# Optimization experiments

Hardware: AMD Instinct MI355X
Metric: run time of the kernel (lower is better)

The kernel has to match this reference:

```python
import jax, jax.numpy as jnp
import numpy as np

H = 16      # num_attention_heads
HKV = 4     # num_key_value_heads
HIDDEN = 1024
HEAD_DIM = HIDDEN // H  # 64
ROPE_BASE = 10000.0


def _rope(x):
    # Rotate-half RoPE applied over the FULL projected last dim, matching the
    # module which applies self._rope before splitting into heads.
    B, S, D = x.shape
    half = D // 2
    inv_freq = 1.0 / (ROPE_BASE ** (jnp.arange(half, dtype=jnp.float32) / half))
    ang = jnp.arange(S, dtype=jnp.float32)[:, None] * inv_freq[None, :]  # [S, half]
    cos, sin = jnp.cos(ang), jnp.sin(ang)
    x1, x2 = x[..., :half], x[..., half:]
    return jnp.concatenate([x1 * cos - x2 * sin, x2 * cos + x1 * sin], axis=-1)


def _rmsnorm(x):
    # F.rms_norm with no weight: x / sqrt(mean(x^2) + eps)
    eps = jnp.finfo(x.dtype).eps
    return x * jax.lax.rsqrt(jnp.mean(x * x, axis=-1, keepdims=True) + eps)


def setup_inputs() -> dict:
    key = jax.random.key(0)
    ks = jax.random.split(key, 10)
    B, S = 2, 2048
    kv_dim = HKV * HEAD_DIM
    sc = 0.02
    return {
        "hidden_state": jax.random.normal(ks[0], (B, S, HIDDEN), dtype=jnp.float32),
        "attention_mask": jnp.zeros((B, S, S), dtype=jnp.float32),
        "Wq": jax.random.normal(ks[1], (HIDDEN, HIDDEN), dtype=jnp.float32) * sc,
        "bq": jnp.zeros((HIDDEN,), dtype=jnp.float32),
        "Wk": jax.random.normal(ks[2], (HIDDEN, kv_dim), dtype=jnp.float32) * sc,
        "bk": jnp.zeros((kv_dim,), dtype=jnp.float32),
        "Wv": jax.random.normal(ks[3], (HIDDEN, kv_dim), dtype=jnp.float32) * sc,
        "bv": jnp.zeros((kv_dim,), dtype=jnp.float32),
        "Wo": jax.random.normal(ks[4], (HIDDEN, HIDDEN), dtype=jnp.float32) * sc,
        "bo": jnp.zeros((HIDDEN,), dtype=jnp.float32),
    }


def reference(hidden_state, attention_mask, Wq, bq, Wk, bk, Wv, bv, Wo, bo):
    B, S, _ = hidden_state.shape
    G = H // HKV  # query heads per kv head
    d = HEAD_DIM

    q = hidden_state @ Wq + bq            # [B,S,H*d]
    k = hidden_state @ Wk + bk            # [B,S,Hkv*d]
    v = hidden_state @ Wv + bv            # [B,S,Hkv*d]

    q = _rope(q)
    k = _rope(k)

    # split heads; repeat_interleave of KV over groups == grouping Q heads as [Hkv, G]
    q = q.reshape(B, S, H, d).transpose(0, 2, 1, 3).reshape(B, HKV, G, S, d)
    k = k.reshape(B, S, HKV, d).transpose(0, 2, 1, 3)   # [B,Hkv,S,d]
    v = v.reshape(B, S, HKV, d).transpose(0, 2, 1, 3)   # [B,Hkv,S,d]

    q = _rmsnorm(q)
    k = _rmsnorm(k)

    scale = d ** 0.5
    scores = jnp.einsum('bkgqd,bksd->bkgqs', q, k) / scale  # [B,Hkv,G,S,S]
    scores = scores + attention_mask[:, None, None, :, :]
    attn = jax.nn.softmax(scores, axis=-1)
    out = jnp.einsum('bkgqs,bksd->bkgqd', attn, v)          # [B,Hkv,G,S,d]

    out = out.reshape(B, H, S, d).transpose(0, 2, 1, 3).reshape(B, S, H * d)
    return out @ Wo + bo
```

## Files before the change

### kernel.cpp

```cpp
#include <hip/hip_runtime.h>
#include <cmath>

#define SEQ 2048
#define BATCH 2
#define HID 1024
#define NH 16
#define NKV 4
#define DH 64
#define KVDIM 256
#define K32C 32

typedef __attribute__((ext_vector_type(8))) short bf16x8;
typedef __attribute__((ext_vector_type(4))) float f32x4;

static __device__ __forceinline__ unsigned short f2bf(float x) {
  union { float f; unsigned u; } v; v.f = x;
  unsigned r = v.u + 0x7fffu + ((v.u >> 16) & 1u);
  return (unsigned short)(r >> 16);
}
static __device__ __forceinline__ float bf2f(unsigned short h) {
  union { unsigned u; float f; } v; v.u = ((unsigned)h) << 16;
  return v.f;
}
static __device__ __forceinline__ void gl_lds16(const unsigned short* g, unsigned short* l) {
  __builtin_amdgcn_global_load_lds(
      (const __attribute__((address_space(1))) unsigned int*)g,
      (__attribute__((address_space(3))) unsigned int*)l, 16, 0, 0);
}

template<bool HILO>
__global__ __launch_bounds__(256) void pack_a_kernel(
    const float* __restrict__ A, unsigned short* __restrict__ hi,
    unsigned short* __restrict__ lo) {
  int gid = blockIdx.x * 256 + threadIdx.x;
  int lane = gid & 63;
  int k32 = (gid >> 6) & 31;
  int m16 = gid >> 11;
  int quad = lane >> 4, l16 = lane & 15;
  const float* src = A + (size_t)(m16 * 16 + l16) * 1024 + k32 * 32 + quad * 8;
  float4 a0 = *(const float4*)src;
  float4 a1 = *(const float4*)(src + 4);
  float v[8] = {a0.x, a0.y, a0.z, a0.w, a1.x, a1.y, a1.z, a1.w};
  unsigned short h[8], l[8];
#pragma unroll
  for (int j = 0; j < 8; ++j) {
    h[j] = f2bf(v[j]);
    if (HILO) l[j] = f2bf(v[j] - bf2f(h[j]));
  }
  *(bf16x8*)(hi + (size_t)gid * 8) = *(bf16x8*)h;
  if (HILO) *(bf16x8*)(lo + (size_t)gid * 8) = *(bf16x8*)l;
}

template<bool HILO>
__global__ __launch_bounds__(256) void pack_b_kernel(
    const float* __restrict__ W, unsigned short* __restrict__ hi,
    unsigned short* __restrict__ lo, int Nsrc) {
  int gid = blockIdx.x * 256 + threadIdx.x;
  int lane = gid & 63;
  int k32 = (gid >> 6) & 31;
  int n16 = gid >> 11;
  int quad = lane >> 4, l16 = lane & 15;
  int n = n16 * 16 + l16, k = k32 * 32 + quad * 8;
  unsigned short h[8], l[8];
#pragma unroll
  for (int j = 0; j < 8; ++j) {
    float v = W[(size_t)(k + j) * Nsrc + n];
    h[j] = f2bf(v);
    if (HILO) l[j] = f2bf(v - bf2f(h[j]));
  }
  *(bf16x8*)(hi + (size_t)gid * 8) = *(bf16x8*)h;
  if (HILO) *(bf16x8*)(lo + (size_t)gid * 8) = *(bf16x8*)l;
}

__global__ __launch_bounds__(256) void bias_cat_kernel(
    const float* __restrict__ bq, const float* __restrict__ bk,
    const float* __restrict__ bv, float* __restrict__ dst) {
  int n = blockIdx.x * 256 + threadIdx.x;
  if (n < 1536)
    dst[n] = (n < 1024) ? bq[n] : (n < 1280 ? bk[n - 1024] : bv[n - 1280]);
}

template<int CHAINS, bool OUTBF16>
__global__ __launch_bounds__(256) void gemm_pk_kernel(
    const unsigned short* __restrict__ Ah, const unsigned short* __restrict__ Al,
    const unsigned short* __restrict__ Bh, const unsigned short* __restrict__ Bl,
    const float* __restrict__ bias, void* __restrict__ Cout, int N) {
  constexpr int NCH = (CHAINS == 3) ? 2 : 1;
  __shared__ unsigned short Asm[NCH][4 * 512];
  __shared__ unsigned short Bsm[NCH][8 * 512];
  const int tid = threadIdx.x;
  const int wave = tid >> 6, lane = tid & 63;
  const int wr = wave >> 1, wc = wave & 1;
  const int quad = lane >> 4, l16 = lane & 15;
  const size_t abase = ((size_t)(blockIdx.y * 4 + wave) * K32C) * 64 + lane;
  const size_t bbase0 = ((size_t)(blockIdx.x * 8 + wave) * K32C) * 64 + lane;
  const size_t bbase1 = ((size_t)(blockIdx.x * 8 + wave + 4) * K32C) * 64 + lane;
  f32x4 acc[2][4] = {};
  for (int k32 = 0; k32 < K32C; ++k32) {
    __syncthreads();
    gl_lds16(Ah + (abase + (size_t)k32 * 64) * 8, &Asm[0][wave * 512]);
    gl_lds16(Bh + (bbase0 + (size_t)k32 * 64) * 8, &Bsm[0][wave * 512]);
    gl_lds16(Bh + (bbase1 + (size_t)k32 * 64) * 8, &Bsm[0][(wave + 4) * 512]);
    if (CHAINS == 3) {
      gl_lds16(Al + (abase + (size_t)k32 * 64) * 8, &Asm[1][wave * 512]);
      gl_lds16(Bl + (bbase0 + (size_t)k32 * 64) * 8, &Bsm[1][wave * 512]);
      gl_lds16(Bl + (bbase1 + (size_t)k32 * 64) * 8, &Bsm[1][(wave + 4) * 512]);
    }
    __syncthreads();
    bf16x8 af[2][NCH], bfr[4][NCH];
#pragma unroll
    for (int mt = 0; mt < 2; ++mt)
#pragma unroll
      for (int ch = 0; ch < NCH; ++ch)
        af[mt][ch] = *(const bf16x8*)&Asm[ch][((wr * 2 + mt) * 64 + lane) * 8];
#pragma unroll
    for (int nt = 0; nt < 4; ++nt)
#pragma unroll
      for (int ch = 0; ch < NCH; ++ch)
        bfr[nt][ch] = *(const bf16x8*)&Bsm[ch][((wc * 4 + nt) * 64 + lane) * 8];
#pragma unroll
    for (int mt = 0; mt < 2; ++mt)
#pragma unroll
      for (int nt = 0; nt < 4; ++nt) {
        acc[mt][nt] = __builtin_amdgcn_mfma_f32_16x16x32_bf16(af[mt][0], bfr[nt][0], acc[mt][nt], 0, 0, 0);
        if (CHAINS == 3) {
          acc[mt][nt] = __builtin_amdgcn_mfma_f32_16x16x32_bf16(af[mt][1], bfr[nt][0], acc[mt][nt], 0, 0, 0);
          acc[mt][nt] = __builtin_amdgcn_mfma_f32_16x16x32_bf16(af[mt][0], bfr[nt][1], acc[mt][nt], 0, 0, 0);
        }
      }
  }
  const int n0 = blockIdx.x * 128 + wc * 64;
  const int m0 = blockIdx.y * 64 + wr * 32;
#pragma unroll
  for (int mt = 0; mt < 2; ++mt)
#pragma unroll
    for (int nt = 0; nt < 4; ++nt)
#pragma unroll
      for (int r = 0; r < 4; ++r) {
        int gm = m0 + mt * 16 + quad * 4 + r;
        int n = n0 + nt * 16 + l16;
        float v = acc[mt][nt][r] + bias[n];
        if (OUTBF16)
          ((unsigned short*)Cout)[(size_t)gm * N + n] = f2bf(v);
        else
          ((float*)Cout)[(size_t)gm * N + n] = v;
      }
}

__global__ __launch_bounds__(1024) void rope_norm_q_kernel(
    const unsigned short* __restrict__ qkv, unsigned short* __restrict__ qnh,
    unsigned short* __restrict__ qnl) {
  const int s = blockIdx.x, b = blockIdx.y;
  const int t = threadIdx.x;
  const unsigned short* row = qkv + ((size_t)b * SEQ + s) * 1536;
  const int j = t & 511;
  float invf = exp2f((float)j * (-13.287712379549449f / 512.0f));
  float ang = (float)s * invf;
  float c = cosf(ang), sn = sinf(ang);
  float x1 = bf2f(row[j]), x2 = bf2f(row[j + 512]);
  float val = (t < 512) ? (x1 * c - x2 * sn) : (x2 * c + x1 * sn);
  float ss = val * val;
#pragma unroll
  for (int off = 1; off < 64; off <<= 1) ss += __shfl_xor(ss, off);
  float rn = rsqrtf(ss * (1.0f / 64.0f) + 1.1920929e-07f);
  float v = val * rn;
  unsigned short hi = f2bf(v);
  unsigned short lo = f2bf(v - bf2f(hi));
  int h = t >> 6, d = t & 63;
  size_t o = (((size_t)b * NH + h) * SEQ + s) * DH + d;
  qnh[o] = hi;
  qnl[o] = lo;
}

__global__ __launch_bounds__(256) void rope_norm_kv_kernel(
    const unsigned short* __restrict__ qkv, unsigned short* __restrict__ knh,
    unsigned short* __restrict__ knl, unsigned short* __restrict__ vt) {
  const int s = blockIdx.x, b = blockIdx.y;
  const int t = threadIdx.x;
  const unsigned short* row = qkv + ((size_t)b * SEQ + s) * 1536;
  const int j = t & 127;
  float invf = exp2f((float)j * (-13.287712379549449f / 128.0f));
  float ang = (float)s * invf;
  float c = cosf(ang), sn = sinf(ang);
  float x1 = bf2f(row[1024 + j]), x2 = bf2f(row[1024 + 128 + j]);
  float val = (t < 128) ? (x1 * c - x2 * sn) : (x2 * c + x1 * sn);
  float ss = val * val;
#pragma unroll
  for (int off = 1; off < 64; off <<= 1) ss += __shfl_xor(ss, off);
  float rn = rsqrtf(ss * (1.0f / 64.0f) + 1.1920929e-07f);
  float kv = val * rn;
  unsigned short hi = f2bf(kv);
  unsigned short lo = f2bf(kv - bf2f(hi));
  int h = t >> 6, d = t & 63;
  size_t o = (((size_t)b * NKV + h) * SEQ + s) * DH + d;
  knh[o] = hi;
  knl[o] = lo;
  vt[(((size_t)b * NKV + h) * DH + d) * SEQ + s] = row[1280 + t];
}

__global__ __launch_bounds__(256) void attn_mfma_kernel(
    const unsigned short* __restrict__ qnh, const unsigned short* __restrict__ qnl,
    const unsigned short* __restrict__ knh, const unsigned short* __restrict__ knl,
    const unsigned short* __restrict__ vtb, const float* __restrict__ mask,
    float* __restrict__ out) {
  __shared__ unsigned short Ksh[32][72];
  __shared__ unsigned short Ksl[32][72];
  __shared__ unsigned short Vts[64][40];
  __shared__ float Ms[32][36];
  __shared__ unsigned short Ps[4][32][40];

  const int b = blockIdx.z, kvh = blockIdx.y;
  const int q0 = blockIdx.x * 32;
  const int tid = threadIdx.x;
  const int wave = tid >> 6, lane = tid & 63;
  const int quad = lane >> 4, l16 = lane & 15;
  const int h = kvh * 4 + wave;

  bf16x8 qh[2][2], ql[2][2];
  {
    const unsigned short* qb_h = qnh + (((size_t)b * NH + h) * SEQ) * DH;
    const unsigned short* qb_l = qnl + (((size_t)b * NH + h) * SEQ) * DH;
#pragma unroll
    for (int mt = 0; mt < 2; ++mt)
#pragma unroll
      for (int kf = 0; kf < 2; ++kf) {
        size_t o = (size_t)(q0 + mt * 16 + l16) * DH + kf * 32 + quad * 8;
        qh[mt][kf] = *(const bf16x8*)(qb_h + o);
        ql[mt][kf] = *(const bf16x8*)(qb_l + o);
      }
  }

  f32x4 O[2][4] = {};
  float l_acc[2][4] = {};

  const unsigned short* Kbh = knh + ((size_t)b * NKV + kvh) * SEQ * DH;
  const unsigned short* Kbl = knl + ((size_t)b * NKV + kvh) * SEQ * DH;
  const unsigned short* Vb  = vtb + ((size_t)b * NKV + kvh) * DH * SEQ;
  const float* mbase = mask + ((size_t)b * SEQ + q0) * SEQ;

  for (int j0 = 0; j0 < SEQ; j0 += 32) {
    __syncthreads();
    {
      int j = tid >> 3, c = tid & 7;
      *(uint4*)&Ksh[j][c * 8] = *(const uint4*)(Kbh + (size_t)(j0 + j) * DH + c * 8);
      *(uint4*)&Ksl[j][c * 8] = *(const uint4*)(Kbl + (size_t)(j0 + j) * DH + c * 8);
      int d = tid >> 2, c2 = tid & 3;
      *(uint4*)&Vts[d][c2 * 8] = *(const uint4*)(Vb + (size_t)d * SEQ + j0 + c2 * 8);
      *(float4*)&Ms[j][c * 4] = *(const float4*)(mbase + (size_t)j * SEQ + j0 + c * 4);
    }
    __syncthreads();

    bf16x8 kbh[2][2], kbl[2][2];
#pragma unroll
    for (int nt = 0; nt < 2; ++nt)
#pragma unroll
      for (int kf = 0; kf < 2; ++kf) {
        kbh[nt][kf] = *(const bf16x8*)&Ksh[nt * 16 + l16][kf * 32 + quad * 8];
        kbl[nt][kf] = *(const bf16x8*)&Ksl[nt * 16 + l16][kf * 32 + quad * 8];
      }

    f32x4 C[2][2] = {};
#pragma unroll
    for (int mt = 0; mt < 2; ++mt)
#pragma unroll
      for (int nt = 0; nt < 2; ++nt) {
#pragma unroll
        for (int kf = 0; kf < 2; ++kf) {
          C[mt][nt] = __builtin_amdgcn_mfma_f32_16x16x32_bf16(qh[mt][kf], kbh[nt][kf], C[mt][nt], 0, 0, 0);
          C[mt][nt] = __builtin_amdgcn_mfma_f32_16x16x32_bf16(ql[mt][kf], kbh[nt][kf], C[mt][nt], 0, 0, 0);
          C[mt][nt] = __builtin_amdgcn_mfma_f32_16x16x32_bf16(qh[mt][kf], kbl[nt][kf], C[mt][nt], 0, 0, 0);
        }
      }

#pragma unroll
    for (int mt = 0; mt < 2; ++mt)
#pragma unroll
      for (int nt = 0; nt < 2; ++nt)
#pragma unroll
        for (int r = 0; r < 4; ++r) {
          int row = mt * 16 + quad * 4 + r;
          float p = __expf(fmaf(C[mt][nt][r], 0.125f, Ms[row][nt * 16 + l16] - 8.0f));
          l_acc[mt][r] += p;
          Ps[wave][row][nt * 16 + l16] = f2bf(p);
        }

    bf16x8 pa[2], vbf[4];
#pragma unroll
    for (int mt = 0; mt < 2; ++mt)
      pa[mt] = *(const bf16x8*)&Ps[wave][mt * 16 + l16][quad * 8];
#pragma unroll
    for (int nt = 0; nt < 4; ++nt)
      vbf[nt] = *(const bf16x8*)&Vts[nt * 16 + l16][quad * 8];
#pragma unroll
    for (int mt = 0; mt < 2; ++mt)
#pragma unroll
      for (int nt = 0; nt < 4; ++nt)
        O[mt][nt] = __builtin_amdgcn_mfma_f32_16x16x32_bf16(pa[mt], vbf[nt], O[mt][nt], 0, 0, 0);
  }

#pragma unroll
  for (int mt = 0; mt < 2; ++mt)
#pragma unroll
    for (int r = 0; r < 4; ++r) {
#pragma unroll
      for (int off = 1; off < 16; off <<= 1)
        l_acc[mt][r] += __shfl_xor(l_acc[mt][r], off);
    }

#pragma unroll
  for (int mt = 0; mt < 2; ++mt)
#pragma unroll
    for (int r = 0; r < 4; ++r) {
      float inv = 1.0f / l_acc[mt][r];
      int s = q0 + mt * 16 + quad * 4 + r;
#pragma unroll
      for (int nt = 0; nt < 4; ++nt)
        out[((size_t)b * SEQ + s) * HID + h * DH + nt * 16 + l16] = O[mt][nt][r] * inv;
    }
}

extern "C" void kernel_launch(void* const* d_in, const int* in_sizes, int n_in,
                              void* d_out, int out_size, void* d_ws, size_t ws_size,
                              hipStream_t stream) {
  const float* hs   = (const float*)d_in[0];
  const float* mask = (const float*)d_in[1];
  const float* Wq   = (const float*)d_in[2];
  const float* bq   = (const float*)d_in[3];
  const float* Wk   = (const float*)d_in[4];
  const float* bk   = (const float*)d_in[5];
  const float* Wv   = (const float*)d_in[6];
  const float* bv   = (const float*)d_in[7];
  const float* Wo   = (const float*)d_in[8];
  const float* bo   = (const float*)d_in[9];
  float* out = (float*)d_out;
  char* ws = (char*)d_ws;
  const size_t MiB = 1048576;

  unsigned short* hs_pk   = (unsigned short*)(ws);
  unsigned short* qkvproj = (unsigned short*)(ws + 8 * MiB);
  float*          attn_o  = (float*)(ws);
  unsigned short* Wqkv_hi = (unsigned short*)(ws + 20 * MiB);
  float*          bias_c  = (float*)(ws + 23 * MiB);
  unsigned short* Wo_hi   = (unsigned short*)(ws + 20 * MiB);
  unsigned short* Wo_lo   = (unsigned short*)(ws + 22 * MiB);
  unsigned short* qnh     = (unsigned short*)(ws + 24 * MiB);
  unsigned short* qnl     = (unsigned short*)(ws + 32 * MiB);
  unsigned short* ao_hi   = (unsigned short*)(ws + 24 * MiB);
  unsigned short* ao_lo   = (unsigned short*)(ws + 32 * MiB);
  unsigned short* knh     = (unsigned short*)(ws + 40 * MiB);
  unsigned short* knl     = (unsigned short*)(ws + 42 * MiB);
  unsigned short* vtb     = (unsigned short*)(ws + 44 * MiB);

  pack_a_kernel<false><<<2048, 256, 0, stream>>>(hs, hs_pk, nullptr);
  pack_b_kernel<false><<<512, 256, 0, stream>>>(Wq, Wqkv_hi, nullptr, 1024);
  pack_b_kernel<false><<<128, 256, 0, stream>>>(Wk, Wqkv_hi + (size_t)64 * 2048 * 8, nullptr, 256);
  pack_b_kernel<false><<<128, 256, 0, stream>>>(Wv, Wqkv_hi + (size_t)80 * 2048 * 8, nullptr, 256);
  bias_cat_kernel<<<6, 256, 0, stream>>>(bq, bk, bv, bias_c);

  gemm_pk_kernel<1, true><<<dim3(12, 64), 256, 0, stream>>>(
      hs_pk, nullptr, Wqkv_hi, nullptr, bias_c, qkvproj, 1536);

  pack_b_kernel<true><<<512, 256, 0, stream>>>(Wo, Wo_hi, Wo_lo, 1024);

  rope_norm_q_kernel<<<dim3(SEQ, BATCH), dim3(1024), 0, stream>>>(qkvproj, qnh, qnl);
  rope_norm_kv_kernel<<<dim3(SEQ, BATCH), dim3(256), 0, stream>>>(qkvproj, knh, knl, vtb);

  attn_mfma_kernel<<<dim3(SEQ / 32, NKV, BATCH), 256, 0, stream>>>(
      qnh, qnl, knh, knl, vtb, mask, attn_o);

  pack_a_kernel<true><<<2048, 256, 0, stream>>>(attn_o, ao_hi, ao_lo);
  gemm_pk_kernel<3, false><<<dim3(8, 64), 256, 0, stream>>>(
      ao_hi, ao_lo, Wo_hi, Wo_lo, bo, out, 1024);
}
```

Measured before the change: 305.0 us.

## Split attention KV range across blocks, pack Q/K/V in MFMA layout, drop K lo term

The attention kernel now splits the key sequence in half across two blocks per head group, doubling the grid, and combines partial outputs and row sums with atomic adds into a zeroed buffer. Final normalization moves into a new pack kernel that divides by the row sum before building the hi/lo split for the output projection. Q, K and V are stored pre-swizzled in MFMA fragment order and loaded with direct global-to-LDS copies. K is kept in bf16 hi only, removing one MFMA per fragment, and the row sum is computed by an MFMA against a ones vector instead of shuffles. In exchange it adds atomics, a memset, and lower precision in the QK product.

```diff
diff --git a/kernel.cpp b/kernel.cpp
--- a/kernel.cpp
+++ b/kernel.cpp
@@ -49,6 +49,34 @@
   }
   *(bf16x8*)(hi + (size_t)gid * 8) = *(bf16x8*)h;
   if (HILO) *(bf16x8*)(lo + (size_t)gid * 8) = *(bf16x8*)l;
+}
+
+__global__ __launch_bounds__(256) void pack_a_norm_kernel(
+    const float* __restrict__ A, const float* __restrict__ lpart,
+    unsigned short* __restrict__ hi, unsigned short* __restrict__ lo) {
+  int gid = blockIdx.x * 256 + threadIdx.x;
+  int lane = gid & 63;
+  int k32 = (gid >> 6) & 31;
+  int m16 = gid >> 11;
+  int quad = lane >> 4, l16 = lane & 15;
+  int m = m16 * 16 + l16;
+  int b = m >> 11, s = m & 2047;
+  int k0 = k32 * 32 + quad * 8;
+  int h = k0 >> 6;
+  float inv = 1.0f / lpart[(size_t)(b * NH + h) * SEQ + s];
+  const float* src = A + (size_t)m * 1024 + k0;
+  float4 a0 = *(const float4*)src;
+  float4 a1 = *(const float4*)(src + 4);
+  float v[8] = {a0.x, a0.y, a0.z, a0.w, a1.x, a1.y, a1.z, a1.w};
+  unsigned short hh[8], ll[8];
+#pragma unroll
+  for (int j = 0; j < 8; ++j) {
+    float x = v[j] * inv;
+    hh[j] = f2bf(x);
+    ll[j] = f2bf(x - bf2f(hh[j]));
+  }
+  *(bf16x8*)(hi + (size_t)gid * 8) = *(bf16x8*)hh;
+  *(bf16x8*)(lo + (size_t)gid * 8) = *(bf16x8*)ll;
 }
 
 template<bool HILO>
@@ -148,8 +176,8 @@
 }
 
 __global__ __launch_bounds__(1024) void rope_norm_q_kernel(
-    const unsigned short* __restrict__ qkv, unsigned short* __restrict__ qnh,
-    unsigned short* __restrict__ qnl) {
+    const unsigned short* __restrict__ qkv, unsigned short* __restrict__ Qh,
+    unsigned short* __restrict__ Ql) {
   const int s = blockIdx.x, b = blockIdx.y;
   const int t = threadIdx.x;
   const unsigned short* row = qkv + ((size_t)b * SEQ + s) * 1536;
@@ -167,14 +195,15 @@
   unsigned short hi = f2bf(v);
   unsigned short lo = f2bf(v - bf2f(hi));
   int h = t >> 6, d = t & 63;
-  size_t o = (((size_t)b * NH + h) * SEQ + s) * DH + d;
-  qnh[o] = hi;
-  qnl[o] = lo;
+  size_t o = (size_t)(b * NH + h) * 131072 +
+             ((((size_t)(s >> 4) * 2 + (d >> 5)) * 64) + ((d >> 3) & 3) * 16 + (s & 15)) * 8 + (d & 7);
+  Qh[o] = hi;
+  Ql[o] = lo;
 }
 
 __global__ __launch_bounds__(256) void rope_norm_kv_kernel(
-    const unsigned short* __restrict__ qkv, unsigned short* __restrict__ knh,
-    unsigned short* __restrict__ knl, unsigned short* __restrict__ vt) {
+    const unsigned short* __restrict__ qkv, unsigned short* __restrict__ Kpk,
+    unsigned short* __restrict__ Vpk) {
   const int s = blockIdx.x, b = blockIdx.y;
   const int t = threadIdx.x;
   const unsigned short* row = qkv + ((size_t)b * SEQ + s) * 1536;
@@ -189,133 +218,126 @@
   for (int off = 1; off < 64; off <<= 1) ss += __shfl_xor(ss, off);
   float rn = rsqrtf(ss * (1.0f / 64.0f) + 1.1920929e-07f);
   float kv = val * rn;
-  unsigned short hi = f2bf(kv);
-  unsigned short lo = f2bf(kv - bf2f(hi));
   int h = t >> 6, d = t & 63;
-  size_t o = (((size_t)b * NKV + h) * SEQ + s) * DH + d;
-  knh[o] = hi;
-  knl[o] = lo;
-  vt[(((size_t)b * NKV + h) * DH + d) * SEQ + s] = row[1280 + t];
-}
-
-__global__ __launch_bounds__(256) void attn_mfma_kernel(
-    const unsigned short* __restrict__ qnh, const unsigned short* __restrict__ qnl,
-    const unsigned short* __restrict__ knh, const unsigned short* __restrict__ knl,
-    const unsigned short* __restrict__ vtb, const float* __restrict__ mask,
-    float* __restrict__ out) {
-  __shared__ unsigned short Ksh[32][72];
-  __shared__ unsigned short Ksl[32][72];
-  __shared__ unsigned short Vts[64][40];
-  __shared__ float Ms[32][36];
-  __shared__ unsigned short Ps[4][32][40];
-
-  const int b = blockIdx.z, kvh = blockIdx.y;
+  size_t ko = (size_t)(b * NKV + h) * 131072 +
+              ((((size_t)(s >> 4) * 2 + (d >> 5)) * 64) + ((d >> 3) & 3) * 16 + (s & 15)) * 8 + (d & 7);
+  Kpk[ko] = f2bf(kv);
+  size_t vo = (size_t)(b * NKV + h) * 131072 +
+              ((((size_t)(d >> 4) * 64 + (s >> 5)) * 64) + ((s >> 3) & 3) * 16 + (d & 15)) * 8 + (s & 7);
+  Vpk[vo] = row[1280 + t];
+}
+
+__global__ __launch_bounds__(256, 4) void attn_mfma2_kernel(
+    const unsigned short* __restrict__ Qh, const unsigned short* __restrict__ Ql,
+    const unsigned short* __restrict__ Kpk, const unsigned short* __restrict__ Vpk,
+    const float* __restrict__ mask, float* __restrict__ attn_po,
+    float* __restrict__ l_part) {
+  __shared__ unsigned short Kb[4 * 512];
+  __shared__ unsigned short Vb[4 * 512];
+  __shared__ float Msk[32][36];
+  __shared__ unsigned short Ps[4][32 * 72];
+
+  const int b = blockIdx.z;
+  const int kvh = blockIdx.y >> 1, jh = blockIdx.y & 1;
   const int q0 = blockIdx.x * 32;
-  const int tid = threadIdx.x;
-  const int wave = tid >> 6, lane = tid & 63;
+  const int tid = threadIdx.x, wave = tid >> 6, lane = tid & 63;
   const int quad = lane >> 4, l16 = lane & 15;
   const int h = kvh * 4 + wave;
 
   bf16x8 qh[2][2], ql[2][2];
   {
-    const unsigned short* qb_h = qnh + (((size_t)b * NH + h) * SEQ) * DH;
-    const unsigned short* qb_l = qnl + (((size_t)b * NH + h) * SEQ) * DH;
+    const unsigned short* Qb_h = Qh + (size_t)(b * NH + h) * 131072;
+    const unsigned short* Qb_l = Ql + (size_t)(b * NH + h) * 131072;
 #pragma unroll
     for (int mt = 0; mt < 2; ++mt)
 #pragma unroll
       for (int kf = 0; kf < 2; ++kf) {
-        size_t o = (size_t)(q0 + mt * 16 + l16) * DH + kf * 32 + quad * 8;
-        qh[mt][kf] = *(const bf16x8*)(qb_h + o);
-        ql[mt][kf] = *(const bf16x8*)(qb_l + o);
+        size_t o = ((((size_t)(q0 >> 4) + mt) * 2 + kf) * 64 + lane) * 8;
+        qh[mt][kf] = *(const bf16x8*)(Qb_h + o);
+        ql[mt][kf] = *(const bf16x8*)(Qb_l + o);
       }
   }
 
+  const unsigned short* Kbase = Kpk + (size_t)(b * NKV + kvh) * 131072;
+  const unsigned short* Vbase = Vpk + (size_t)(b * NKV + kvh) * 131072;
+
+  bf16x8 ones;
+#pragma unroll
+  for (int i = 0; i < 8; ++i) ones[i] = (short)0x3F80;
+
   f32x4 O[2][4] = {};
-  float l_acc[2][4] = {};
-
-  const unsigned short* Kbh = knh + ((size_t)b * NKV + kvh) * SEQ * DH;
-  const unsigned short* Kbl = knl + ((size_t)b * NKV + kvh) * SEQ * DH;
-  const unsigned short* Vb  = vtb + ((size_t)b * NKV + kvh) * DH * SEQ;
-  const float* mbase = mask + ((size_t)b * SEQ + q0) * SEQ;
-
-  for (int j0 = 0; j0 < SEQ; j0 += 32) {
+  f32x4 lAcc[2] = {};
+
+  const int jbase = jh * (SEQ / 2);
+  for (int jc = 0; jc < 32; ++jc) {
+    const int j0 = jbase + jc * 32;
     __syncthreads();
     {
-      int j = tid >> 3, c = tid & 7;
-      *(uint4*)&Ksh[j][c * 8] = *(const uint4*)(Kbh + (size_t)(j0 + j) * DH + c * 8);
-      *(uint4*)&Ksl[j][c * 8] = *(const uint4*)(Kbl + (size_t)(j0 + j) * DH + c * 8);
-      int d = tid >> 2, c2 = tid & 3;
-      *(uint4*)&Vts[d][c2 * 8] = *(const uint4*)(Vb + (size_t)d * SEQ + j0 + c2 * 8);
-      *(float4*)&Ms[j][c * 4] = *(const float4*)(mbase + (size_t)j * SEQ + j0 + c * 4);
+      gl_lds16(Kbase + ((((size_t)(j0 >> 4) + (wave >> 1)) * 2 + (wave & 1)) * 64 + lane) * 8,
+               &Kb[wave * 512]);
+      gl_lds16(Vbase + (((size_t)wave * 64 + (j0 >> 5)) * 64 + lane) * 8,
+               &Vb[wave * 512]);
+      int mr = tid >> 3, c4 = tid & 7;
+      float4 m4 = *(const float4*)(mask + ((size_t)b * SEQ + q0 + mr) * SEQ + j0 + c4 * 4);
+      Msk[mr][c4 * 4 + 0] = m4.x - 8.0f;
+      Msk[mr][c4 * 4 + 1] = m4.y - 8.0f;
+      Msk[mr][c4 * 4 + 2] = m4.z - 8.0f;
+      Msk[mr][c4 * 4 + 3] = m4.w - 8.0f;
     }
     __syncthreads();
 
-    bf16x8 kbh[2][2], kbl[2][2];
+    bf16x8 kbf[2][2], vbf[4];
 #pragma unroll
     for (int nt = 0; nt < 2; ++nt)
 #pragma unroll
-      for (int kf = 0; kf < 2; ++kf) {
-        kbh[nt][kf] = *(const bf16x8*)&Ksh[nt * 16 + l16][kf * 32 + quad * 8];
-        kbl[nt][kf] = *(const bf16x8*)&Ksl[nt * 16 + l16][kf * 32 + quad * 8];
-      }
-
-    f32x4 C[2][2] = {};
+      for (int kf = 0; kf < 2; ++kf)
+        kbf[nt][kf] = *(const bf16x8*)&Kb[((nt * 2 + kf) * 64 + lane) * 8];
+#pragma unroll
+    for (int d16 = 0; d16 < 4; ++d16)
+      vbf[d16] = *(const bf16x8*)&Vb[(d16 * 64 + lane) * 8];
+
 #pragma unroll
     for (int mt = 0; mt < 2; ++mt)
 #pragma unroll
       for (int nt = 0; nt < 2; ++nt) {
-#pragma unroll
-        for (int kf = 0; kf < 2; ++kf) {
-          C[mt][nt] = __builtin_amdgcn_mfma_f32_16x16x32_bf16(qh[mt][kf], kbh[nt][kf], C[mt][nt], 0, 0, 0);
-          C[mt][nt] = __builtin_amdgcn_mfma_f32_16x16x32_bf16(ql[mt][kf], kbh[nt][kf], C[mt][nt], 0, 0, 0);
-          C[mt][nt] = __builtin_amdgcn_mfma_f32_16x16x32_bf16(qh[mt][kf], kbl[nt][kf], C[mt][nt], 0, 0, 0);
+        f32x4 C = {};
+        C = __builtin_amdgcn_mfma_f32_16x16x32_bf16(qh[mt][0], kbf[nt][0], C, 0, 0, 0);
+        C = __builtin_amdgcn_mfma_f32_16x16x32_bf16(qh[mt][1], kbf[nt][1], C, 0, 0, 0);
+        C = __builtin_amdgcn_mfma_f32_16x16x32_bf16(ql[mt][0], kbf[nt][0], C, 0, 0, 0);
+        C = __builtin_amdgcn_mfma_f32_16x16x32_bf16(ql[mt][1], kbf[nt][1], C, 0, 0, 0);
+#pragma unroll
+        for (int r = 0; r < 4; ++r) {
+          int row = mt * 16 + quad * 4 + r;
+          float p = __expf(fmaf(C[r], 0.125f, Msk[row][nt * 16 + l16]));
+          union { float f; unsigned u; } pu; pu.f = p;
+          Ps[wave][row * 72 + nt * 16 + l16] = (unsigned short)((pu.u + 0x8000u) >> 16);
         }
       }
 
-#pragma unroll
-    for (int mt = 0; mt < 2; ++mt)
-#pragma unroll
-      for (int nt = 0; nt < 2; ++nt)
-#pragma unroll
-        for (int r = 0; r < 4; ++r) {
-          int row = mt * 16 + quad * 4 + r;
-          float p = __expf(fmaf(C[mt][nt][r], 0.125f, Ms[row][nt * 16 + l16] - 8.0f));
-          l_acc[mt][r] += p;
-          Ps[wave][row][nt * 16 + l16] = f2bf(p);
-        }
-
-    bf16x8 pa[2], vbf[4];
-#pragma unroll
-    for (int mt = 0; mt < 2; ++mt)
-      pa[mt] = *(const bf16x8*)&Ps[wave][mt * 16 + l16][quad * 8];
-#pragma unroll
-    for (int nt = 0; nt < 4; ++nt)
-      vbf[nt] = *(const bf16x8*)&Vts[nt * 16 + l16][quad * 8];
-#pragma unroll
-    for (int mt = 0; mt < 2; ++mt)
+    bf16x8 pa[2];
+#pragma unroll
+    for (int mt = 0; mt < 2; ++mt)
+      pa[mt] = *(const bf16x8*)&Ps[wave][(mt * 16 + l16) * 72 + quad * 8];
+#pragma unroll
+    for (int mt = 0; mt < 2; ++mt) {
+      lAcc[mt] = __builtin_amdgcn_mfma_f32_16x16x32_bf16(pa[mt], ones, lAcc[mt], 0, 0, 0);
 #pragma unroll
       for (int nt = 0; nt < 4; ++nt)
         O[mt][nt] = __builtin_amdgcn_mfma_f32_16x16x32_bf16(pa[mt], vbf[nt], O[mt][nt], 0, 0, 0);
+    }
   }
 
 #pragma unroll
   for (int mt = 0; mt < 2; ++mt)
 #pragma unroll
     for (int r = 0; r < 4; ++r) {
-#pragma unroll
-      for (int off = 1; off < 16; off <<= 1)
-        l_acc[mt][r] += __shfl_xor(l_acc[mt][r], off);
-    }
-
-#pragma unroll
-  for (int mt = 0; mt < 2; ++mt)
-#pragma unroll
-    for (int r = 0; r < 4; ++r) {
-      float inv = 1.0f / l_acc[mt][r];
       int s = q0 + mt * 16 + quad * 4 + r;
 #pragma unroll
       for (int nt = 0; nt < 4; ++nt)
-        out[((size_t)b * SEQ + s) * HID + h * DH + nt * 16 + l16] = O[mt][nt][r] * inv;
+        atomicAdd(attn_po + ((size_t)b * SEQ + s) * HID + h * DH + nt * 16 + l16,
+                  O[mt][nt][r]);
+      if (l16 == 0)
+        atomicAdd(l_part + (size_t)(b * NH + h) * SEQ + s, lAcc[mt][r]);
     }
 }
 
@@ -338,18 +360,18 @@
 
   unsigned short* hs_pk   = (unsigned short*)(ws);
   unsigned short* qkvproj = (unsigned short*)(ws + 8 * MiB);
-  float*          attn_o  = (float*)(ws);
+  float*          attn_po = (float*)(ws);
+  float*          l_part  = (float*)(ws + 16 * MiB);
   unsigned short* Wqkv_hi = (unsigned short*)(ws + 20 * MiB);
-  float*          bias_c  = (float*)(ws + 23 * MiB);
   unsigned short* Wo_hi   = (unsigned short*)(ws + 20 * MiB);
   unsigned short* Wo_lo   = (unsigned short*)(ws + 22 * MiB);
-  unsigned short* qnh     = (unsigned short*)(ws + 24 * MiB);
-  unsigned short* qnl     = (unsigned short*)(ws + 32 * MiB);
+  unsigned short* Qpk_h   = (unsigned short*)(ws + 24 * MiB);
+  unsigned short* Qpk_l   = (unsigned short*)(ws + 32 * MiB);
   unsigned short* ao_hi   = (unsigned short*)(ws + 24 * MiB);
   unsigned short* ao_lo   = (unsigned short*)(ws + 32 * MiB);
-  unsigned short* knh     = (unsigned short*)(ws + 40 * MiB);
-  unsigned short* knl     = (unsigned short*)(ws + 42 * MiB);
-  unsigned short* vtb     = (unsigned short*)(ws + 44 * MiB);
+  unsigned short* Kpk     = (unsigned short*)(ws + 40 * MiB);
+  unsigned short* Vpk     = (unsigned short*)(ws + 42 * MiB);
+  float*          bias_c  = (float*)(ws + 44 * MiB);
 
   pack_a_kernel<false><<<2048, 256, 0, stream>>>(hs, hs_pk, nullptr);
   pack_b_kernel<false><<<512, 256, 0, stream>>>(Wq, Wqkv_hi, nullptr, 1024);
@@ -362,13 +384,14 @@
 
   pack_b_kernel<true><<<512, 256, 0, stream>>>(Wo, Wo_hi, Wo_lo, 1024);
 
-  rope_norm_q_kernel<<<dim3(SEQ, BATCH), dim3(1024), 0, stream>>>(qkvproj, qnh, qnl);
-  rope_norm_kv_kernel<<<dim3(SEQ, BATCH), dim3(256), 0, stream>>>(qkvproj, knh, knl, vtb);
-
-  attn_mfma_kernel<<<dim3(SEQ / 32, NKV, BATCH), 256, 0, stream>>>(
-      qnh, qnl, knh, knl, vtb, mask, attn_o);
-
-  pack_a_kernel<true><<<2048, 256, 0, stream>>>(attn_o, ao_hi, ao_lo);
+  rope_norm_q_kernel<<<dim3(SEQ, BATCH), dim3(1024), 0, stream>>>(qkvproj, Qpk_h, Qpk_l);
+  rope_norm_kv_kernel<<<dim3(SEQ, BATCH), dim3(256), 0, stream>>>(qkvproj, Kpk, Vpk);
+
+  hipMemsetAsync(ws, 0, 16 * MiB + 262144, stream);
+  attn_mfma2_kernel<<<dim3(SEQ / 32, NKV * 2, BATCH), 256, 0, stream>>>(
+      Qpk_h, Qpk_l, Kpk, Vpk, mask, attn_po, l_part);
+
+  pack_a_norm_kernel<<<2048, 256, 0, stream>>>(attn_po, l_part, ao_hi, ao_lo);
   gemm_pk_kernel<3, false><<<dim3(8, 64), 256, 0, stream>>>(
       ao_hi, ao_lo, Wo_hi, Wo_lo, bo, out, 1024);
 }
```

New measurement: 285.6 us. 6.3% less time.
